# Performance work log

Hardware: AMD Instinct MI355X
Metric: run time of the kernel (lower is better)

## Reference

```python
import jax, jax.numpy as jnp
import numpy as np
import math

NUM_HEADS = 8

def _ln(x, g, b, eps=1e-5):
    mu = x.mean(-1, keepdims=True)
    var = ((x - mu) ** 2).mean(-1, keepdims=True)
    return (x - mu) / jnp.sqrt(var + eps) * g + b

def setup_inputs() -> dict:
    key = jax.random.key(0)
    ks = jax.random.split(key, 10)
    B, Nq, Nk, dQ, dK, dV = 16, 1024, 1024, 512, 512, 512
    s = 0.05  # small init so the double-exp in masked_softmax stays finite
    Q = jax.random.normal(ks[0], (B, Nq, dQ), jnp.float32)
    K = jax.random.normal(ks[1], (B, Nk, dK), jnp.float32)
    Qm = (jax.random.uniform(ks[2], (B, Nq, 1)) < 0.9).astype(jnp.float32)
    Km = (jax.random.uniform(ks[3], (B, Nk, 1)) < 0.9).astype(jnp.float32)
    Wq = jax.random.normal(ks[4], (dQ, dV), jnp.float32) * s
    Wk = jax.random.normal(ks[5], (dK, dV), jnp.float32) * s
    Wv = jax.random.normal(ks[6], (dK, dV), jnp.float32) * s
    Wo = jax.random.normal(ks[7], (dV, dV), jnp.float32) * s
    bq = jnp.zeros((dV,), jnp.float32); bk = jnp.zeros((dV,), jnp.float32)
    bv = jnp.zeros((dV,), jnp.float32); bo = jnp.zeros((dV,), jnp.float32)
    g0 = jnp.ones((dV,), jnp.float32); b0 = jnp.zeros((dV,), jnp.float32)
    g1 = jnp.ones((dV,), jnp.float32); b1 = jnp.zeros((dV,), jnp.float32)
    return {"Q": Q, "K": K, "Qm": Qm, "Km": Km,
            "Wq": Wq, "bq": bq, "Wk": Wk, "bk": bk, "Wv": Wv, "bv": bv,
            "Wo": Wo, "bo": bo, "g0": g0, "b0": b0, "g1": g1, "b1": b1}

def reference(Q, K, Qm, Km, Wq, bq, Wk, bk, Wv, bv, Wo, bo, g0, b0, g1, b1):
    B, Nq, _ = Q.shape
    Nk = K.shape[1]
    dV = Wq.shape[1]
    h = NUM_HEADS
    dh = dV // h
    # projections + feature masking (Qm/Km broadcast over feature dim)
    Qp = (Q @ Wq + bq) * Qm          # [B,Nq,dV]
    Kp = (K @ Wk + bk) * Km          # [B,Nk,dV]
    V  = K @ Wv + bv                 # [B,Nk,dV]
    # head split: torch.cat(split(dh,2),0) == head-major [h,B,N,dh]
    Qh = Qp.reshape(B, Nq, h, dh).transpose(2, 0, 1, 3)
    Kh = Kp.reshape(B, Nk, h, dh).transpose(2, 0, 1, 3)
    Vh = V.reshape(B, Nk, h, dh).transpose(2, 0, 1, 3)
    S = jnp.einsum('hbqd,hbkd->hbqk', Qh, Kh) / math.sqrt(dV)
    # faithful masked_softmax: exp applied twice (Km branch then Qm branch)
    X = jnp.exp(S) * Km[:, :, 0][None, :, None, :]   # [h,B,Nq,Nk]
    X = jnp.exp(X) * Qm[:, :, 0][None, :, :, None]
    A = X / (X.sum(-1, keepdims=True) + 1e-8)
    O = Qh + jnp.einsum('hbqk,hbkd->hbqd', A, Vh)    # residual in head space
    O = O.transpose(1, 2, 0, 3).reshape(B, Nq, dV)   # merge heads back
    O = _ln(O, g0, b0)
    O = O + jax.nn.relu(O @ Wo + bo)
    return _ln(O, g1, b1)
```

## Files before the change

### kernel.cpp

```cpp
#include <hip/hip_runtime.h>
#include <hip/hip_bf16.h>
#include <cstdint>


typedef __bf16 bf16;
typedef __bf16 bf16x4 __attribute__((ext_vector_type(4)));
typedef __bf16 bf16x8 __attribute__((ext_vector_type(8)));
typedef float f32x4 __attribute__((ext_vector_type(4)));

#define MFMA16(a, b, c) __builtin_amdgcn_mfma_f32_16x16x32_bf16((a), (b), (c), 0, 0, 0)

#if __has_builtin(__builtin_amdgcn_exp2f)
#define EXP2F(x) __builtin_amdgcn_exp2f(x)
#else
#define EXP2F(x) exp2f(x)
#endif

static __device__ __forceinline__ void async_lds16(const bf16* g, bf16* l) {
  __builtin_amdgcn_global_load_lds(
      (__attribute__((address_space(1))) void*)(void*)g,
      (__attribute__((address_space(3))) void*)l,
      16, 0, 0);
}

static __device__ __forceinline__ void swz512(int id, long& rowBase, int& colBase) {
  colBase = ((id >> 3) & 3) * 128;
  rowBase = (long)((id & 7) + 8 * (id >> 5)) * 128;
}

struct ConvArgs {
  const float* src[10];
  bf16* dst[10];
  int n[10];
};

__global__ __launch_bounds__(256) void prep(
    const float* __restrict__ Wq, const float* __restrict__ Wk,
    const float* __restrict__ Wv, const float* __restrict__ Wo,
    bf16* __restrict__ Tq, bf16* __restrict__ Tk,
    bf16* __restrict__ Tv, bf16* __restrict__ To, ConvArgs ca) {
  __shared__ bf16 t[64][72];
  const int id = blockIdx.x;
  const int tid = threadIdx.x;
  if (id < 256) {
    const int bx = id & 7, by = (id >> 3) & 7, bz = id >> 6;
    const float* src;
    bf16* dst;
    switch (bz) {
      case 0: src = Wq; dst = Tq; break;
      case 1: src = Wk; dst = Tk; break;
      case 2: src = Wv; dst = Tv; break;
      default: src = Wo; dst = To; break;
    }
    const int n0 = bx * 64;
    const int k0 = by * 64;
    for (int c = tid; c < 512; c += 256) {
      const int row = c >> 3, col = (c & 7) * 8;
      const float* sp = src + (size_t)(k0 + row) * 512 + n0 + col;
      const f32x4 a = *(const f32x4*)sp;
      const f32x4 b = *(const f32x4*)(sp + 4);
      bf16x8 v;
#pragma unroll
      for (int j = 0; j < 4; ++j) { v[j] = (bf16)a[j]; v[j + 4] = (bf16)b[j]; }
      *(bf16x8*)(&t[row][col]) = v;
    }
    __syncthreads();
    for (int c = tid; c < 512; c += 256) {
      const int row = c >> 3, col8 = (c & 7) * 8;
      bf16x8 v;
#pragma unroll
      for (int j = 0; j < 8; ++j) v[j] = t[col8 + j][row];
      *(bf16x8*)(dst + (size_t)(n0 + row) * 512 + k0 + col8) = v;
    }
  } else {
    const int cid = id - 256;
    const int seg = cid >> 3;
    const int n = ca.n[seg];
    const long i = ((long)(cid & 7) * 256 + tid) * 8;
    if (i >= n) return;
    const float* s = ca.src[seg];
    const f32x4 x0 = *(const f32x4*)(s + i);
    const f32x4 x1 = *(const f32x4*)(s + i + 4);
    bf16x8 o;
#pragma unroll
    for (int j = 0; j < 4; ++j) { o[j] = (bf16)x0[j]; o[j + 4] = (bf16)x1[j]; }
    *(bf16x8*)(ca.dst[seg] + i) = o;
  }
}

__global__ __launch_bounds__(256, 2) void gemm512(
    const bf16* __restrict__ A, const bf16* __restrict__ Bt,
    const bf16* __restrict__ bias, const bf16* __restrict__ mask,
    const bf16* __restrict__ resid, bf16* __restrict__ out) {
  __shared__ bf16 sA[128 * 32];
  __shared__ bf16 sB[128 * 32];
  const int tid = threadIdx.x;
  const int lane = tid & 63;
  const int w = tid >> 6;
  const int fm = lane & 15;
  const int fq = lane >> 4;
  long rowBase; int colBase;
  swz512(blockIdx.x, rowBase, colBase);

  f32x4 acc[4][4] = {};

  const int c0 = tid, c1 = tid + 256;
  const int r0 = c0 >> 2, o0 = (c0 & 3) * 8;
  const int r1 = c1 >> 2, o1 = (c1 & 3) * 8;
  const bf16* A0 = A + (rowBase + r0) * 512 + o0;
  const bf16* A1 = A + (rowBase + r1) * 512 + o1;
  const bf16* B0 = Bt + (size_t)(colBase + r0) * 512 + o0;
  const bf16* B1 = Bt + (size_t)(colBase + r1) * 512 + o1;

  const int wr = (w & 1) * 64;
  const int wc = (w >> 1) * 64;

  for (int kt = 0; kt < 16; ++kt) {
    const int k0 = kt * 32;
    __syncthreads();
    async_lds16(A0 + k0, sA + c0 * 8);
    async_lds16(A1 + k0, sA + c1 * 8);
    async_lds16(B0 + k0, sB + c0 * 8);
    async_lds16(B1 + k0, sB + c1 * 8);
    __syncthreads();
    bf16x8 a[4], b[4];
#pragma unroll
    for (int i = 0; i < 4; ++i)
      a[i] = *(const bf16x8*)(sA + (wr + i * 16 + fm) * 32 + fq * 8);
#pragma unroll
    for (int j = 0; j < 4; ++j)
      b[j] = *(const bf16x8*)(sB + (wc + j * 16 + fm) * 32 + fq * 8);
#pragma unroll
    for (int i = 0; i < 4; ++i)
#pragma unroll
      for (int j = 0; j < 4; ++j)
        acc[i][j] = MFMA16(a[i], b[j], acc[i][j]);
  }

#pragma unroll
  for (int i = 0; i < 4; ++i) {
#pragma unroll
    for (int r = 0; r < 4; ++r) {
      const long R = rowBase + wr + i * 16 + fq * 4 + r;
      const float mk = mask ? (float)mask[R] : 1.0f;
      const bf16* resrow = resid ? resid + R * 512 : nullptr;
      bf16* outrow = out + R * 512;
#pragma unroll
      for (int j = 0; j < 4; ++j) {
        const int C = colBase + wc + j * 16 + fm;
        float v = acc[i][j][r] + (float)bias[C];
        if (mask) v *= mk;
        if (resid) v = (float)resrow[C] + fmaxf(v, 0.0f);
        outrow[C] = (bf16)v;
      }
    }
  }
}

__global__ __launch_bounds__(256, 2) void proj_all(
    const float* __restrict__ Qf, const float* __restrict__ Kf,
    const bf16* __restrict__ Tq, const bf16* __restrict__ Tk,
    const bf16* __restrict__ Tv, const bf16* __restrict__ bq,
    const bf16* __restrict__ bk, const bf16* __restrict__ bv,
    const bf16* __restrict__ Qm, const bf16* __restrict__ Km,
    bf16* __restrict__ Qp, bf16* __restrict__ Kp, bf16* __restrict__ Vt) {
  __shared__ bf16 sA[128 * 32];
  __shared__ bf16 sB1[128 * 32];
  __shared__ bf16 sB2[128 * 32];
  const int tid = threadIdx.x;
  const int lane = tid & 63;
  const int w = tid >> 6;
  const int fm = lane & 15;
  const int fq = lane >> 4;
  const int wr = (w & 1) * 64;
  const int wc = (w >> 1) * 64;
  const int c0 = tid, c1 = tid + 256;
  const int r0 = c0 >> 2, o0 = (c0 & 3) * 8;
  const int r1 = c1 >> 2, o1 = (c1 & 3) * 8;

  if (blockIdx.x < 512) {
    long rowBase; int colBase;
    swz512(blockIdx.x, rowBase, colBase);
    f32x4 acc[4][4] = {};
    const float* A0 = Qf + (rowBase + r0) * 512 + o0;
    const float* A1 = Qf + (rowBase + r1) * 512 + o1;
    const bf16* B0 = Tq + (size_t)(colBase + r0) * 512 + o0;
    const bf16* B1 = Tq + (size_t)(colBase + r1) * 512 + o1;

    f32x4 x0 = *(const f32x4*)(A0);
    f32x4 x1 = *(const f32x4*)(A0 + 4);
    f32x4 y0 = *(const f32x4*)(A1);
    f32x4 y1 = *(const f32x4*)(A1 + 4);

    for (int kt = 0; kt < 16; ++kt) {
      __syncthreads();
      async_lds16(B0 + kt * 32, sB1 + c0 * 8);
      async_lds16(B1 + kt * 32, sB1 + c1 * 8);
      {
        bf16x8 va, vb;
#pragma unroll
        for (int j = 0; j < 4; ++j) {
          va[j] = (bf16)x0[j]; va[j + 4] = (bf16)x1[j];
          vb[j] = (bf16)y0[j]; vb[j + 4] = (bf16)y1[j];
        }
        *(bf16x8*)(sA + c0 * 8) = va;
        *(bf16x8*)(sA + c1 * 8) = vb;
      }
      __syncthreads();
      if (kt < 15) {
        const int k1 = kt * 32 + 32;
        x0 = *(const f32x4*)(A0 + k1);
        x1 = *(const f32x4*)(A0 + k1 + 4);
        y0 = *(const f32x4*)(A1 + k1);
        y1 = *(const f32x4*)(A1 + k1 + 4);
      }
      bf16x8 a[4], b[4];
#pragma unroll
      for (int i = 0; i < 4; ++i)
        a[i] = *(const bf16x8*)(sA + (wr + i * 16 + fm) * 32 + fq * 8);
#pragma unroll
      for (int j = 0; j < 4; ++j)
        b[j] = *(const bf16x8*)(sB1 + (wc + j * 16 + fm) * 32 + fq * 8);
#pragma unroll
      for (int i = 0; i < 4; ++i)
#pragma unroll
        for (int j = 0; j < 4; ++j)
          acc[i][j] = MFMA16(a[i], b[j], acc[i][j]);
    }

#pragma unroll
    for (int i = 0; i < 4; ++i) {
#pragma unroll
      for (int r = 0; r < 4; ++r) {
        const long R = rowBase + wr + i * 16 + fq * 4 + r;
        const float mk = (float)Qm[R];
        bf16* outrow = Qp + R * 512;
#pragma unroll
        for (int j = 0; j < 4; ++j) {
          const int C = colBase + wc + j * 16 + fm;
          outrow[C] = (bf16)((acc[i][j][r] + (float)bq[C]) * mk);
        }
      }
    }
  } else {
    long rowBase; int colBase;
    swz512(blockIdx.x - 512, rowBase, colBase);
    f32x4 acck[4][4] = {};
    f32x4 accv[4][4] = {};
    const float* A0 = Kf + (rowBase + r0) * 512 + o0;
    const float* A1 = Kf + (rowBase + r1) * 512 + o1;
    const bf16* Bk0 = Tk + (size_t)(colBase + r0) * 512 + o0;
    const bf16* Bk1 = Tk + (size_t)(colBase + r1) * 512 + o1;
    const bf16* Bv0 = Tv + (size_t)(colBase + r0) * 512 + o0;
    const bf16* Bv1 = Tv + (size_t)(colBase + r1) * 512 + o1;

    f32x4 x0 = *(const f32x4*)(A0);
    f32x4 x1 = *(const f32x4*)(A0 + 4);
    f32x4 y0 = *(const f32x4*)(A1);
    f32x4 y1 = *(const f32x4*)(A1 + 4);

    for (int kt = 0; kt < 16; ++kt) {
      const int k0 = kt * 32;
      __syncthreads();
      async_lds16(Bk0 + k0, sB1 + c0 * 8);
      async_lds16(Bk1 + k0, sB1 + c1 * 8);
      async_lds16(Bv0 + k0, sB2 + c0 * 8);
      async_lds16(Bv1 + k0, sB2 + c1 * 8);
      {
        bf16x8 va, vb;
#pragma unroll
        for (int j = 0; j < 4; ++j) {
          va[j] = (bf16)x0[j]; va[j + 4] = (bf16)x1[j];
          vb[j] = (bf16)y0[j]; vb[j + 4] = (bf16)y1[j];
        }
        *(bf16x8*)(sA + c0 * 8) = va;
        *(bf16x8*)(sA + c1 * 8) = vb;
      }
      __syncthreads();
      if (kt < 15) {
        const int k1 = k0 + 32;
        x0 = *(const f32x4*)(A0 + k1);
        x1 = *(const f32x4*)(A0 + k1 + 4);
        y0 = *(const f32x4*)(A1 + k1);
        y1 = *(const f32x4*)(A1 + k1 + 4);
      }
      bf16x8 a[4], b[4], bv2[4];
#pragma unroll
      for (int i = 0; i < 4; ++i)
        a[i] = *(const bf16x8*)(sA + (wr + i * 16 + fm) * 32 + fq * 8);
#pragma unroll
      for (int j = 0; j < 4; ++j) {
        b[j] = *(const bf16x8*)(sB1 + (wc + j * 16 + fm) * 32 + fq * 8);
        bv2[j] = *(const bf16x8*)(sB2 + (wc + j * 16 + fm) * 32 + fq * 8);
      }
#pragma unroll
      for (int i = 0; i < 4; ++i)
#pragma unroll
        for (int j = 0; j < 4; ++j) {
          acck[i][j] = MFMA16(a[i], b[j], acck[i][j]);
          accv[i][j] = MFMA16(a[i], bv2[j], accv[i][j]);
        }
    }

    const int bidx = (int)(rowBase >> 10);
#pragma unroll
    for (int i = 0; i < 4; ++i) {
#pragma unroll
      for (int r = 0; r < 4; ++r) {
        const long R = rowBase + wr + i * 16 + fq * 4 + r;
        const int rs = (int)(R & 7) << 3;
        const float mk = (float)Km[R];
        bf16* outrow = Kp + R * 512;
#pragma unroll
        for (int j = 0; j < 4; ++j) {
          const int C = colBase + wc + j * 16 + fm;
          const int Cs = (C & ~63) | ((C & 63) ^ rs);
          outrow[Cs] = (bf16)((acck[i][j][r] + (float)bk[C]) * mk);
        }
      }
      const int kkb = (int)(rowBase & 1023) + wr + i * 16 + fq * 4;
#pragma unroll
      for (int j = 0; j < 4; ++j) {
        const int C = colBase + wc + j * 16 + fm;
        const int ds = (C & 7) << 3;
        const int kks = (kkb & ~63) | ((kkb & 63) ^ ds);
        const float bvc = (float)bv[C];
        bf16x4 pv;
#pragma unroll
        for (int r = 0; r < 4; ++r) pv[r] = (bf16)(accv[i][j][r] + bvc);
        bf16* dst =
            Vt + ((size_t)(bidx * 8 + (C >> 6)) * 64 + (C & 63)) * 1024 + kks;
        *(bf16x4*)((void*)dst) = pv;
      }
    }
  }
}

__global__ __launch_bounds__(256, 3) void attn_kernel(
    bf16* __restrict__ Qp, const bf16* __restrict__ Kp,
    const bf16* __restrict__ Vt, const bf16* __restrict__ Qm,
    const bf16* __restrict__ Km) {
  __shared__ bf16 sK[2][64][64];
  __shared__ bf16 sVt[2][64][64];
  __shared__ bf16 sX[4][32][72];
  __shared__ bf16 sKm[1024];
  __shared__ float sL[4][32];

  const int tid = threadIdx.x;
  const int lane = tid & 63;
  const int w = tid >> 6;
  const int fm = lane & 15;
  const int fq = lane >> 4;
  const int id = blockIdx.x;
  const int bh = id & 127;
  const int q0 = (id >> 7) * 128;
  const int b = bh >> 3;
  const int hh = bh & 7;
  const int rot = (id >> 3) & 15;

  bf16* Qbase = Qp + ((long)b * 1024 + q0) * 512 + hh * 64;
  float qm_lane[2];
  qm_lane[0] = (float)Qm[(long)b * 1024 + q0 + w * 32 + fm];
  qm_lane[1] = (float)Qm[(long)b * 1024 + q0 + w * 32 + 16 + fm];

  bf16x8 qf[2][2];
#pragma unroll
  for (int u = 0; u < 2; ++u)
#pragma unroll
    for (int ks = 0; ks < 2; ++ks)
      qf[u][ks] = *(const bf16x8*)(Qbase + (long)(w * 32 + u * 16 + fm) * 512 +
                                   ks * 32 + fq * 8);

  f32x4 acc_o[2][4] = {};
  float l_lane[2] = {0.f, 0.f};
  const float c1 = 0.063758715f;
  const float C2 = 0.5287663729448977f;

  const bf16* Vthead = Vt + ((long)b * 8 + hh) * 64 * 1024;
  const bf16* Kbb = Kp + (long)b * 1024 * 512 + hh * 64;
  const bf16* Kmb = Km + (long)b * 1024;

  const int srow = tid >> 3;
  const int scol = (tid & 7) * 8;
  const int xsw = (fm & 7) << 3;

  {
    const int kk0 = (rot & 15) * 64;
    const bf16* Kb0 = Kbb + (long)kk0 * 512;
    async_lds16(Kb0 + (long)srow * 512 + scol, &sK[0][0][0] + tid * 8);
    async_lds16(Kb0 + (long)(srow + 32) * 512 + scol,
                &sK[0][0][0] + 2048 + tid * 8);
    async_lds16(Vthead + (long)srow * 1024 + kk0 + scol, &sVt[0][0][0] + tid * 8);
    async_lds16(Vthead + (long)(srow + 32) * 1024 + kk0 + scol,
                &sVt[0][0][0] + 2048 + tid * 8);
    *(bf16x4*)(&sKm[tid * 4]) = *(const bf16x4*)(Kmb + tid * 4);
  }
  __syncthreads();

  for (int kt = 0; kt < 16; ++kt) {
    const int cur = kt & 1;
    if (kt < 15) {
      const int kk1 = ((kt + 1 + rot) & 15) * 64;
      const bf16* Kb1 = Kbb + (long)kk1 * 512;
      bf16* dK = &sK[cur ^ 1][0][0];
      bf16* dV = &sVt[cur ^ 1][0][0];
      async_lds16(Kb1 + (long)srow * 512 + scol, dK + tid * 8);
      async_lds16(Kb1 + (long)(srow + 32) * 512 + scol, dK + 2048 + tid * 8);
      async_lds16(Vthead + (long)srow * 1024 + kk1 + scol, dV + tid * 8);
      async_lds16(Vthead + (long)(srow + 32) * 1024 + kk1 + scol,
                  dV + 2048 + tid * 8);
    }
    const int kkT = ((kt + rot) & 15) * 64;

    f32x4 s_acc[2][4] = {};
#pragma unroll
    for (int ks = 0; ks < 2; ++ks) {
      const int kc = (ks * 32 + fq * 8) ^ xsw;
#pragma unroll
      for (int t = 0; t < 4; ++t) {
        const bf16x8 kf = *(const bf16x8*)(&sK[cur][t * 16 + fm][kc]);
        s_acc[0][t] = MFMA16(kf, qf[0][ks], s_acc[0][t]);
        s_acc[1][t] = MFMA16(kf, qf[1][ks], s_acc[1][t]);
      }
    }
#pragma unroll
    for (int t = 0; t < 4; ++t) {
      const bf16x4 km4 = *(const bf16x4*)(&sKm[kkT + t * 16 + fq * 4]);
      float kmf[4];
#pragma unroll
      for (int r = 0; r < 4; ++r) kmf[r] = (float)km4[r];
#pragma unroll
      for (int u = 0; u < 2; ++u) {
        bf16x4 xp;
#pragma unroll
        for (int r = 0; r < 4; ++r) {
          const float e1L = EXP2F(fmaf(s_acc[u][t][r], c1, C2));
          const float y = EXP2F(e1L * kmf[r]);
          l_lane[u] += y;
          xp[r] = (bf16)y;
        }
        *(bf16x4*)((void*)&sX[w][u * 16 + fm][t * 16 + fq * 4]) = xp;
      }
    }
#pragma unroll
    for (int ks = 0; ks < 2; ++ks) {
      const int kc = (ks * 32 + fq * 8) ^ xsw;
      const bf16x8 xf0 = *(const bf16x8*)(&sX[w][fm][ks * 32 + fq * 8]);
      const bf16x8 xf1 = *(const bf16x8*)(&sX[w][16 + fm][ks * 32 + fq * 8]);
#pragma unroll
      for (int t = 0; t < 4; ++t) {
        const bf16x8 vf = *(const bf16x8*)(&sVt[cur][t * 16 + fm][kc]);
        acc_o[0][t] = MFMA16(xf0, vf, acc_o[0][t]);
        acc_o[1][t] = MFMA16(xf1, vf, acc_o[1][t]);
      }
    }
    __syncthreads();
  }

#pragma unroll
  for (int u = 0; u < 2; ++u) {
    l_lane[u] += __shfl_xor(l_lane[u], 16);
    l_lane[u] += __shfl_xor(l_lane[u], 32);
    if (fq == 0) sL[w][u * 16 + fm] = l_lane[u];
  }
  __syncthreads();

#pragma unroll
  for (int u = 0; u < 2; ++u) {
#pragma unroll
    for (int t = 0; t < 4; ++t) {
#pragma unroll
      for (int r = 0; r < 4; ++r) {
        const int qr = w * 32 + u * 16 + fq * 4 + r;
        const int dc = t * 16 + fm;
        const float qm_r = __shfl(qm_lane[u], fq * 4 + r, 64);
        const float li = 1.0f / (qm_r * sL[w][u * 16 + fq * 4 + r] + 1e-8f);
        const float val =
            (float)Qbase[(long)qr * 512 + dc] + qm_r * acc_o[u][t][r] * li;
        Qbase[(long)qr * 512 + dc] = (bf16)val;
      }
    }
  }
}

__global__ __launch_bounds__(256) void lnorm(
    const bf16* __restrict__ X, const bf16* __restrict__ g,
    const bf16* __restrict__ bb, bf16* __restrict__ out) {
  const int row = blockIdx.x * 4 + (threadIdx.x >> 6);
  const int lane = threadIdx.x & 63;
  const bf16x8 v = *(const bf16x8*)(X + (size_t)row * 512 + lane * 8);
  float x[8], s = 0.f, ss = 0.f;
#pragma unroll
  for (int j = 0; j < 8; ++j) {
    x[j] = (float)v[j];
    s += x[j];
    ss += x[j] * x[j];
  }
#pragma unroll
  for (int m = 1; m < 64; m <<= 1) {
    s += __shfl_xor(s, m);
    ss += __shfl_xor(ss, m);
  }
  const float mean = s * (1.0f / 512.0f);
  const float var = ss * (1.0f / 512.0f) - mean * mean;
  const float rstd = 1.0f / sqrtf(var + 1e-5f);
  const bf16x8 gv = *(const bf16x8*)(g + lane * 8);
  const bf16x8 bv = *(const bf16x8*)(bb + lane * 8);
  bf16x8 o;
#pragma unroll
  for (int j = 0; j < 8; ++j)
    o[j] = (bf16)((x[j] - mean) * rstd * (float)gv[j] + (float)bv[j]);
  *(bf16x8*)(out + (size_t)row * 512 + lane * 8) = o;
}

__global__ __launch_bounds__(256) void lnorm_out(
    const bf16* __restrict__ X, const bf16* __restrict__ g,
    const bf16* __restrict__ bb, float* __restrict__ out) {
  const int row = blockIdx.x * 4 + (threadIdx.x >> 6);
  const int lane = threadIdx.x & 63;
  const bf16x8 v = *(const bf16x8*)(X + (size_t)row * 512 + lane * 8);
  float x[8], s = 0.f, ss = 0.f;
#pragma unroll
  for (int j = 0; j < 8; ++j) {
    x[j] = (float)v[j];
    s += x[j];
    ss += x[j] * x[j];
  }
#pragma unroll
  for (int m = 1; m < 64; m <<= 1) {
    s += __shfl_xor(s, m);
    ss += __shfl_xor(ss, m);
  }
  const float mean = s * (1.0f / 512.0f);
  const float var = ss * (1.0f / 512.0f) - mean * mean;
  const float rstd = 1.0f / sqrtf(var + 1e-5f);
  const bf16x8 gv = *(const bf16x8*)(g + lane * 8);
  const bf16x8 bv = *(const bf16x8*)(bb + lane * 8);
  f32x4 a, c;
#pragma unroll
  for (int j = 0; j < 4; ++j) {
    a[j] = (x[j] - mean) * rstd * (float)gv[j] + (float)bv[j];
    c[j] = (x[j + 4] - mean) * rstd * (float)gv[j + 4] + (float)bv[j + 4];
  }
  float* fo = out + (size_t)row * 512 + lane * 8;
  *(f32x4*)fo = a;
  *(f32x4*)(fo + 4) = c;
}

extern "C" void kernel_launch(void* const* d_in, const int* in_sizes, int n_in,
                              void* d_out, int out_size, void* d_ws, size_t ws_size,
                              hipStream_t stream) {
  (void)in_sizes; (void)n_in; (void)out_size; (void)ws_size;
  const float* Q = (const float*)d_in[0];
  const float* K = (const float*)d_in[1];

  bf16* ws = (bf16*)d_ws;
  const long W2 = 512L * 512;
  const long MN = 16384L * 512;
  bf16* Tq = ws;
  bf16* Tk = Tq + W2;
  bf16* Tv = Tk + W2;
  bf16* To = Tv + W2;
  bf16* sm = To + W2;
  bf16* cQm = sm + 8 * 512;
  bf16* cKm = cQm + 16384;
  bf16* Qp = cKm + 16384;
  bf16* Kp = Qp + MN;
  bf16* Vt = (bf16*)d_out + MN;

  bf16* cbq = sm + 0 * 512;
  bf16* cbk = sm + 1 * 512;
  bf16* cbv = sm + 2 * 512;
  bf16* cbo = sm + 3 * 512;
  bf16* cg0 = sm + 4 * 512;
  bf16* cb0 = sm + 5 * 512;
  bf16* cg1 = sm + 6 * 512;
  bf16* cb1 = sm + 7 * 512;

  ConvArgs ca;
  ca.src[0] = (const float*)d_in[2];  ca.dst[0] = cQm; ca.n[0] = 16384;
  ca.src[1] = (const float*)d_in[3];  ca.dst[1] = cKm; ca.n[1] = 16384;
  ca.src[2] = (const float*)d_in[5];  ca.dst[2] = cbq; ca.n[2] = 512;
  ca.src[3] = (const float*)d_in[7];  ca.dst[3] = cbk; ca.n[3] = 512;
  ca.src[4] = (const float*)d_in[9];  ca.dst[4] = cbv; ca.n[4] = 512;
  ca.src[5] = (const float*)d_in[11]; ca.dst[5] = cbo; ca.n[5] = 512;
  ca.src[6] = (const float*)d_in[12]; ca.dst[6] = cg0; ca.n[6] = 512;
  ca.src[7] = (const float*)d_in[13]; ca.dst[7] = cb0; ca.n[7] = 512;
  ca.src[8] = (const float*)d_in[14]; ca.dst[8] = cg1; ca.n[8] = 512;
  ca.src[9] = (const float*)d_in[15]; ca.dst[9] = cb1; ca.n[9] = 512;

  prep<<<336, 256, 0, stream>>>(
      (const float*)d_in[4], (const float*)d_in[6],
      (const float*)d_in[8], (const float*)d_in[10], Tq, Tk, Tv, To, ca);

  proj_all<<<1024, 256, 0, stream>>>(Q, K, Tq, Tk, Tv, cbq, cbk, cbv,
                                     cQm, cKm, Qp, Kp, Vt);

  attn_kernel<<<1024, 256, 0, stream>>>(Qp, Kp, Vt, cQm, cKm);

  lnorm<<<4096, 256, 0, stream>>>(Qp, cg0, cb0, Qp);
  gemm512<<<512, 256, 0, stream>>>(Qp, To, cbo, nullptr, Qp, Kp);
  lnorm_out<<<4096, 256, 0, stream>>>(Kp, cg1, cb1, (float*)d_out);
}
```

Measured before the change: 281.8 us.

## Double-buffer LDS tiles in output GEMM and projection kernels

Converts the gemm512 and proj_all main loops to double-buffered shared memory. The next K-tile's async global-to-LDS loads (and, in proj_all, the fp32-to-bf16 A conversion and store) are issued before computing on the current buffer. This drops one barrier per iteration and overlaps memory latency with MFMA work. In exchange it doubles LDS per block, which may limit occupancy, and relies on the async LDS writes completing by the next barrier.

After: 286.3 us. About the same (+1.6%).

```diff
diff --git a/kernel.cpp b/kernel.cpp
--- a/kernel.cpp
+++ b/kernel.cpp
@@ -92,8 +92,8 @@
     const bf16* __restrict__ A, const bf16* __restrict__ Bt,
     const bf16* __restrict__ bias, const bf16* __restrict__ mask,
     const bf16* __restrict__ resid, bf16* __restrict__ out) {
-  __shared__ bf16 sA[128 * 32];
-  __shared__ bf16 sB[128 * 32];
+  __shared__ bf16 sA[2][128 * 32];
+  __shared__ bf16 sB[2][128 * 32];
   const int tid = threadIdx.x;
   const int lane = tid & 63;
   const int w = tid >> 6;
@@ -115,26 +115,34 @@
   const int wr = (w & 1) * 64;
   const int wc = (w >> 1) * 64;
 
+  async_lds16(A0, sA[0] + c0 * 8);
+  async_lds16(A1, sA[0] + c1 * 8);
+  async_lds16(B0, sB[0] + c0 * 8);
+  async_lds16(B1, sB[0] + c1 * 8);
+  __syncthreads();
+
   for (int kt = 0; kt < 16; ++kt) {
-    const int k0 = kt * 32;
-    __syncthreads();
-    async_lds16(A0 + k0, sA + c0 * 8);
-    async_lds16(A1 + k0, sA + c1 * 8);
-    async_lds16(B0 + k0, sB + c0 * 8);
-    async_lds16(B1 + k0, sB + c1 * 8);
-    __syncthreads();
+    const int cur = kt & 1;
+    if (kt < 15) {
+      const int k1 = (kt + 1) * 32;
+      async_lds16(A0 + k1, sA[cur ^ 1] + c0 * 8);
+      async_lds16(A1 + k1, sA[cur ^ 1] + c1 * 8);
+      async_lds16(B0 + k1, sB[cur ^ 1] + c0 * 8);
+      async_lds16(B1 + k1, sB[cur ^ 1] + c1 * 8);
+    }
     bf16x8 a[4], b[4];
 #pragma unroll
     for (int i = 0; i < 4; ++i)
-      a[i] = *(const bf16x8*)(sA + (wr + i * 16 + fm) * 32 + fq * 8);
+      a[i] = *(const bf16x8*)(sA[cur] + (wr + i * 16 + fm) * 32 + fq * 8);
 #pragma unroll
     for (int j = 0; j < 4; ++j)
-      b[j] = *(const bf16x8*)(sB + (wc + j * 16 + fm) * 32 + fq * 8);
+      b[j] = *(const bf16x8*)(sB[cur] + (wc + j * 16 + fm) * 32 + fq * 8);
 #pragma unroll
     for (int i = 0; i < 4; ++i)
 #pragma unroll
       for (int j = 0; j < 4; ++j)
         acc[i][j] = MFMA16(a[i], b[j], acc[i][j]);
+    __syncthreads();
   }
 
 #pragma unroll
@@ -164,9 +172,7 @@
     const bf16* __restrict__ bk, const bf16* __restrict__ bv,
     const bf16* __restrict__ Qm, const bf16* __restrict__ Km,
     bf16* __restrict__ Qp, bf16* __restrict__ Kp, bf16* __restrict__ Vt) {
-  __shared__ bf16 sA[128 * 32];
-  __shared__ bf16 sB1[128 * 32];
-  __shared__ bf16 sB2[128 * 32];
+  __shared__ bf16 smem[24576];
   const int tid = threadIdx.x;
   const int lane = tid & 63;
   const int w = tid >> 6;
@@ -186,46 +192,69 @@
     const float* A1 = Qf + (rowBase + r1) * 512 + o1;
     const bf16* B0 = Tq + (size_t)(colBase + r0) * 512 + o0;
     const bf16* B1 = Tq + (size_t)(colBase + r1) * 512 + o1;
-
-    f32x4 x0 = *(const f32x4*)(A0);
-    f32x4 x1 = *(const f32x4*)(A0 + 4);
-    f32x4 y0 = *(const f32x4*)(A1);
-    f32x4 y1 = *(const f32x4*)(A1 + 4);
-
-    for (int kt = 0; kt < 16; ++kt) {
-      __syncthreads();
-      async_lds16(B0 + kt * 32, sB1 + c0 * 8);
-      async_lds16(B1 + kt * 32, sB1 + c1 * 8);
-      {
-        bf16x8 va, vb;
-#pragma unroll
-        for (int j = 0; j < 4; ++j) {
-          va[j] = (bf16)x0[j]; va[j + 4] = (bf16)x1[j];
-          vb[j] = (bf16)y0[j]; vb[j + 4] = (bf16)y1[j];
-        }
-        *(bf16x8*)(sA + c0 * 8) = va;
-        *(bf16x8*)(sA + c1 * 8) = vb;
-      }
-      __syncthreads();
-      if (kt < 15) {
-        const int k1 = kt * 32 + 32;
-        x0 = *(const f32x4*)(A0 + k1);
-        x1 = *(const f32x4*)(A0 + k1 + 4);
-        y0 = *(const f32x4*)(A1 + k1);
-        y1 = *(const f32x4*)(A1 + k1 + 4);
-      }
+    bf16* bufA[2] = {smem, smem + 4096};
+    bf16* bufB[2] = {smem + 8192, smem + 12288};
+
+    auto loadA = [&](int t, f32x4& u0, f32x4& u1, f32x4& v0, f32x4& v1) {
+      const int k = t * 32;
+      u0 = *(const f32x4*)(A0 + k);
+      u1 = *(const f32x4*)(A0 + k + 4);
+      v0 = *(const f32x4*)(A1 + k);
+      v1 = *(const f32x4*)(A1 + k + 4);
+    };
+    auto writeA = [&](bf16* dst, const f32x4& u0, const f32x4& u1,
+                      const f32x4& v0, const f32x4& v1) {
+      bf16x8 va, vb;
+#pragma unroll
+      for (int j = 0; j < 4; ++j) {
+        va[j] = (bf16)u0[j]; va[j + 4] = (bf16)u1[j];
+        vb[j] = (bf16)v0[j]; vb[j + 4] = (bf16)v1[j];
+      }
+      *(bf16x8*)(dst + c0 * 8) = va;
+      *(bf16x8*)(dst + c1 * 8) = vb;
+    };
+    auto stageB = [&](int t, int bb) {
+      const int k = t * 32;
+      async_lds16(B0 + k, bufB[bb] + c0 * 8);
+      async_lds16(B1 + k, bufB[bb] + c1 * 8);
+    };
+    auto compute = [&](int bb) {
       bf16x8 a[4], b[4];
 #pragma unroll
       for (int i = 0; i < 4; ++i)
-        a[i] = *(const bf16x8*)(sA + (wr + i * 16 + fm) * 32 + fq * 8);
+        a[i] = *(const bf16x8*)(bufA[bb] + (wr + i * 16 + fm) * 32 + fq * 8);
 #pragma unroll
       for (int j = 0; j < 4; ++j)
-        b[j] = *(const bf16x8*)(sB1 + (wc + j * 16 + fm) * 32 + fq * 8);
+        b[j] = *(const bf16x8*)(bufB[bb] + (wc + j * 16 + fm) * 32 + fq * 8);
 #pragma unroll
       for (int i = 0; i < 4; ++i)
 #pragma unroll
         for (int j = 0; j < 4; ++j)
           acc[i][j] = MFMA16(a[i], b[j], acc[i][j]);
+    };
+
+    f32x4 aX0, aX1, aY0, aY1;
+    f32x4 bX0, bX1, bY0, bY1;
+    loadA(0, aX0, aX1, aY0, aY1);
+    writeA(bufA[0], aX0, aX1, aY0, aY1);
+    stageB(0, 0);
+    loadA(1, bX0, bX1, bY0, bY1);
+    __syncthreads();
+
+    for (int kt2 = 0; kt2 < 8; ++kt2) {
+      const int kt = kt2 * 2;
+      stageB(kt + 1, 1);
+      writeA(bufA[1], bX0, bX1, bY0, bY1);
+      if (kt + 2 < 16) loadA(kt + 2, aX0, aX1, aY0, aY1);
+      compute(0);
+      __syncthreads();
+      if (kt + 2 < 16) {
+        stageB(kt + 2, 0);
+        writeA(bufA[0], aX0, aX1, aY0, aY1);
+        if (kt + 3 < 16) loadA(kt + 3, bX0, bX1, bY0, bY1);
+      }
+      compute(1);
+      __syncthreads();
     }
 
 #pragma unroll
@@ -253,53 +282,76 @@
     const bf16* Bk1 = Tk + (size_t)(colBase + r1) * 512 + o1;
     const bf16* Bv0 = Tv + (size_t)(colBase + r0) * 512 + o0;
     const bf16* Bv1 = Tv + (size_t)(colBase + r1) * 512 + o1;
-
-    f32x4 x0 = *(const f32x4*)(A0);
-    f32x4 x1 = *(const f32x4*)(A0 + 4);
-    f32x4 y0 = *(const f32x4*)(A1);
-    f32x4 y1 = *(const f32x4*)(A1 + 4);
-
-    for (int kt = 0; kt < 16; ++kt) {
-      const int k0 = kt * 32;
-      __syncthreads();
-      async_lds16(Bk0 + k0, sB1 + c0 * 8);
-      async_lds16(Bk1 + k0, sB1 + c1 * 8);
-      async_lds16(Bv0 + k0, sB2 + c0 * 8);
-      async_lds16(Bv1 + k0, sB2 + c1 * 8);
-      {
-        bf16x8 va, vb;
-#pragma unroll
-        for (int j = 0; j < 4; ++j) {
-          va[j] = (bf16)x0[j]; va[j + 4] = (bf16)x1[j];
-          vb[j] = (bf16)y0[j]; vb[j + 4] = (bf16)y1[j];
-        }
-        *(bf16x8*)(sA + c0 * 8) = va;
-        *(bf16x8*)(sA + c1 * 8) = vb;
-      }
-      __syncthreads();
-      if (kt < 15) {
-        const int k1 = k0 + 32;
-        x0 = *(const f32x4*)(A0 + k1);
-        x1 = *(const f32x4*)(A0 + k1 + 4);
-        y0 = *(const f32x4*)(A1 + k1);
-        y1 = *(const f32x4*)(A1 + k1 + 4);
-      }
-      bf16x8 a[4], b[4], bv2[4];
+    bf16* bufA[2] = {smem, smem + 4096};
+    bf16* bufBk[2] = {smem + 8192, smem + 12288};
+    bf16* bufBv[2] = {smem + 16384, smem + 20480};
+
+    auto loadA = [&](int t, f32x4& u0, f32x4& u1, f32x4& v0, f32x4& v1) {
+      const int k = t * 32;
+      u0 = *(const f32x4*)(A0 + k);
+      u1 = *(const f32x4*)(A0 + k + 4);
+      v0 = *(const f32x4*)(A1 + k);
+      v1 = *(const f32x4*)(A1 + k + 4);
+    };
+    auto writeA = [&](bf16* dst, const f32x4& u0, const f32x4& u1,
+                      const f32x4& v0, const f32x4& v1) {
+      bf16x8 va, vb;
+#pragma unroll
+      for (int j = 0; j < 4; ++j) {
+        va[j] = (bf16)u0[j]; va[j + 4] = (bf16)u1[j];
+        vb[j] = (bf16)v0[j]; vb[j + 4] = (bf16)v1[j];
+      }
+      *(bf16x8*)(dst + c0 * 8) = va;
+      *(bf16x8*)(dst + c1 * 8) = vb;
+    };
+    auto stageB = [&](int t, int bb) {
+      const int k = t * 32;
+      async_lds16(Bk0 + k, bufBk[bb] + c0 * 8);
+      async_lds16(Bk1 + k, bufBk[bb] + c1 * 8);
+      async_lds16(Bv0 + k, bufBv[bb] + c0 * 8);
+      async_lds16(Bv1 + k, bufBv[bb] + c1 * 8);
+    };
+    auto compute = [&](int bb) {
+      bf16x8 a[4], b[4], b2[4];
 #pragma unroll
       for (int i = 0; i < 4; ++i)
-        a[i] = *(const bf16x8*)(sA + (wr + i * 16 + fm) * 32 + fq * 8);
+        a[i] = *(const bf16x8*)(bufA[bb] + (wr + i * 16 + fm) * 32 + fq * 8);
 #pragma unroll
       for (int j = 0; j < 4; ++j) {
-        b[j] = *(const bf16x8*)(sB1 + (wc + j * 16 + fm) * 32 + fq * 8);
-        bv2[j] = *(const bf16x8*)(sB2 + (wc + j * 16 + fm) * 32 + fq * 8);
+        b[j] = *(const bf16x8*)(bufBk[bb] + (wc + j * 16 + fm) * 32 + fq * 8);
+        b2[j] = *(const bf16x8*)(bufBv[bb] + (wc + j * 16 + fm) * 32 + fq * 8);
       }
 #pragma unroll
       for (int i = 0; i < 4; ++i)
 #pragma unroll
         for (int j = 0; j < 4; ++j) {
           acck[i][j] = MFMA16(a[i], b[j], acck[i][j]);
-          accv[i][j] = MFMA16(a[i], bv2[j], accv[i][j]);
+          accv[i][j] = MFMA16(a[i], b2[j], accv[i][j]);
         }
+    };
+
+    f32x4 aX0, aX1, aY0, aY1;
+    f32x4 bX0, bX1, bY0, bY1;
+    loadA(0, aX0, aX1, aY0, aY1);
+    writeA(bufA[0], aX0, aX1, aY0, aY1);
+    stageB(0, 0);
+    loadA(1, bX0, bX1, bY0, bY1);
+    __syncthreads();
+
+    for (int kt2 = 0; kt2 < 8; ++kt2) {
+      const int kt = kt2 * 2;
+      stageB(kt + 1, 1);
+      writeA(bufA[1], bX0, bX1, bY0, bY1);
+      if (kt + 2 < 16) loadA(kt + 2, aX0, aX1, aY0, aY1);
+      compute(0);
+      __syncthreads();
+      if (kt + 2 < 16) {
+        stageB(kt + 2, 0);
+        writeA(bufA[0], aX0, aX1, aY0, aY1);
+        if (kt + 3 < 16) loadA(kt + 3, bX0, bX1, bY0, bY1);
+      }
+      compute(1);
+      __syncthreads();
     }
 
     const int bidx = (int)(rowBase >> 10);
```
